# Optimization experiments

Hardware: AMD Instinct MI355X
Metric: run time of the kernel (lower is better)

Reference implementation:

```python
import jax, jax.numpy as jnp
import numpy as np
from jax import lax

KERNEL = 3
SAMPLING_RATE = 100.0
N_GRID = 201  # np.linspace(-1, 1, 201) sub-sample grid


def setup_inputs() -> dict:
    key = jax.random.key(0)
    nb, nc, nx, nt = 32, 3, 64, 4096
    xcorr = jax.random.normal(key, (nb, nc, nx, nt), dtype=jnp.float32)
    return {"xcorr": xcorr, "nlag": nt // 2}


def reference(xcorr, nlag):
    nt = xcorr.shape[-1]
    x = jnp.abs(xcorr)  # vabs=True

    # max_pool2d with (1, kernel=3), stride 1, padding (0, 1) -> SAME max over lag axis
    smax = lax.reduce_window(
        x, -jnp.inf, lax.max,
        window_dimensions=(1, 1, 1, KERNEL),
        window_strides=(1, 1, 1, 1),
        padding=[(0, 0), (0, 0), (0, 0), (KERNEL // 2, KERNEL // 2)],
    )
    keep = (smax == x).astype(x.dtype)

    # top-2 local maxima along lag axis (sorted descending, like torch.topk)
    topk_score, topk_idx = lax.top_k(x * keep, 2)
    s0 = topk_score[..., 0]
    s1 = topk_score[..., 1]
    weight = (0.1 + 3.0 * (s0 - s1)) * s0 ** 2
    i0 = topk_idx[..., 0]  # [nb, nc, nx]

    # --- sub-sample interpolation: 3-point spline == parabola through neighbors ---
    offsets = jnp.array([-1, 0, 1], dtype=i0.dtype)
    nbr_idx = jnp.clip(i0[..., None] + offsets, 0, nt - 1)      # [nb,nc,nx,3]
    y = jnp.take_along_axis(x, nbr_idx, axis=-1)                 # [nb,nc,nx,3]
    ym1, y0, yp1 = y[..., 0], y[..., 1], y[..., 2]
    a = 0.5 * (ym1 + yp1) - y0   # quadratic coeff
    b = 0.5 * (yp1 - ym1)        # linear coeff
    c = y0                       # constant

    xg = jnp.linspace(-1.0, 1.0, N_GRID, dtype=x.dtype)          # [201]
    yg = (a[..., None] * xg + b[..., None]) * xg + c[..., None]  # [nb,nc,nx,201]
    ii = jnp.argmax(yg, axis=-1)                                  # [nb,nc,nx]
    sub_shift = xg[ii]
    topk_idx_f = i0.astype(x.dtype) + sub_shift
    topk_score0 = jnp.take_along_axis(yg, ii[..., None], axis=-1)[..., 0]

    # pick the channel with the largest weight
    idx = jnp.argmax(weight, axis=1, keepdims=True)               # [nb,1,nx]
    max_cc = jnp.take_along_axis(topk_score0, idx, axis=1)
    w = jnp.take_along_axis(weight, idx, axis=1)
    shift_idx = jnp.take_along_axis(topk_idx_f, idx, axis=1) - jnp.asarray(nlag, x.dtype)
    shift_t = shift_idx / SAMPLING_RATE

    # stacked: [cc_max, cc_weight, cc_dt, cc_shift], each [nb,1,nx]
    return jnp.stack([max_cc, w, shift_t, shift_idx], axis=0)
```

## Files before the change

### kernel.cpp

```cpp
#include <hip/hip_runtime.h>
#include <math.h>

#define NB 32
#define NC 3
#define NX 64
#define NT 4096
#define NROWS (NB * NC * NX)
#define NGRID 201

__device__ __forceinline__ bool better(float va, int ia, float vb, int ib) {
    return (va > vb) || (va == vb && ia < ib);
}

__global__ __launch_bounds__(256) void row_peaks_kernel(
    const float* __restrict__ xcorr,
    float* __restrict__ w_out,
    float* __restrict__ s_out,
    float* __restrict__ f_out)
{
    __shared__ float xs[NT];
    __shared__ float rv0[4], rv1[4];
    __shared__ int   ri0[4], ri1[4];

    const int row = blockIdx.x;
    const int tid = threadIdx.x;
    const float* __restrict__ xr = xcorr + (size_t)row * NT;

    #pragma unroll
    for (int it = 0; it < NT / 1024; ++it) {
        const int e = it * 1024 + tid * 4;
        float4 v = *reinterpret_cast<const float4*>(xr + e);
        xs[e + 0] = fabsf(v.x);
        xs[e + 1] = fabsf(v.y);
        xs[e + 2] = fabsf(v.z);
        xs[e + 3] = fabsf(v.w);
    }
    __syncthreads();

    float v0 = -1.0f, v1 = -1.0f;
    int   i0 = 0x7fffffff, i1 = 0x7fffffff;
    #pragma unroll
    for (int it = 0; it < NT / 256; ++it) {
        const int t = it * 256 + tid;
        const float c = xs[t];
        const float l = (t > 0)      ? xs[t - 1] : -INFINITY;
        const float r = (t < NT - 1) ? xs[t + 1] : -INFINITY;
        const float v = (c >= l && c >= r) ? c : 0.0f;
        if (v > v0)      { v1 = v0; i1 = i0; v0 = v; i0 = t; }
        else if (v > v1) { v1 = v;  i1 = t; }
    }

    #pragma unroll
    for (int off = 1; off < 64; off <<= 1) {
        const float ov0 = __shfl_xor(v0, off);
        const int   oi0 = __shfl_xor(i0, off);
        const float ov1 = __shfl_xor(v1, off);
        const int   oi1 = __shfl_xor(i1, off);
        if (better(ov0, oi0, v0, i0)) {
            float nv1; int ni1;
            if (better(v0, i0, ov1, oi1)) { nv1 = v0;  ni1 = i0;  }
            else                          { nv1 = ov1; ni1 = oi1; }
            v0 = ov0; i0 = oi0; v1 = nv1; i1 = ni1;
        } else {
            if (better(ov0, oi0, v1, i1)) { v1 = ov0; i1 = oi0; }
        }
    }

    const int wid = tid >> 6;
    if ((tid & 63) == 0) { rv0[wid] = v0; ri0[wid] = i0; rv1[wid] = v1; ri1[wid] = i1; }
    __syncthreads();

    if (tid < 64) {
        float a0 = rv0[0], a1 = rv1[0];
        int   ai0 = ri0[0], ai1 = ri1[0];
        #pragma unroll
        for (int w = 1; w < 4; ++w) {
            const float b0 = rv0[w], b1 = rv1[w];
            const int   bi0 = ri0[w], bi1 = ri1[w];
            if (better(b0, bi0, a0, ai0)) {
                float nv1; int ni1;
                if (better(a0, ai0, b1, bi1)) { nv1 = a0; ni1 = ai0; }
                else                          { nv1 = b1; ni1 = bi1; }
                a0 = b0; ai0 = bi0; a1 = nv1; ai1 = ni1;
            } else {
                if (better(b0, bi0, a1, ai1)) { a1 = b0; ai1 = bi0; }
            }
        }

        const float s0 = a0, s1 = a1;
        const int   p0 = ai0;
        const float s0sq   = s0 * s0;
        const float weight = (0.1f + 3.0f * (s0 - s1)) * s0sq;

        const int im1 = (p0 - 1 < 0) ? 0 : p0 - 1;
        const int ip1 = (p0 + 1 > NT - 1) ? NT - 1 : p0 + 1;
        const float ym1 = xs[im1], yc = xs[p0], yp1 = xs[ip1];
        const float A = 0.5f * (ym1 + yp1) - yc;
        const float B = 0.5f * (yp1 - ym1);
        const float C = yc;

        float bv = -INFINITY; int bi = 0x7fffffff;
        #pragma unroll
        for (int k = 0; k < 4; ++k) {
            const int gi = tid + k * 64;
            if (gi < NGRID) {
                const float xg = 0.01f * (float)(gi - 100);
                const float yg = (A * xg + B) * xg + C;
                if (yg > bv) { bv = yg; bi = gi; }
            }
        }
        #pragma unroll
        for (int off = 1; off < 64; off <<= 1) {
            const float ov = __shfl_xor(bv, off);
            const int   oi = __shfl_xor(bi, off);
            if (ov > bv || (ov == bv && oi < bi)) { bv = ov; bi = oi; }
        }

        if (tid == 0) {
            const float sub = 0.01f * (float)(bi - 100);
            w_out[row] = weight;
            s_out[row] = bv;
            f_out[row] = (float)p0 + sub;
        }
    }
}

__global__ __launch_bounds__(256) void select_channel_kernel(
    const float* __restrict__ w_in,
    const float* __restrict__ s_in,
    const float* __restrict__ f_in,
    const int*   __restrict__ nlag_p,
    float* __restrict__ out)
{
    const int idx = blockIdx.x * blockDim.x + threadIdx.x;
    const int n = NB * NX;
    if (idx >= n) return;
    const int b = idx / NX;
    const int x = idx % NX;

    const float nlagf = (float)(*nlag_p);

    float bw = -INFINITY; int bc = 0;
    #pragma unroll
    for (int c = 0; c < NC; ++c) {
        const float wc = w_in[(b * NC + c) * NX + x];
        if (wc > bw) { bw = wc; bc = c; }
    }
    const int rsel = (b * NC + bc) * NX + x;
    const float mc = s_in[rsel];
    const float shift_idx = f_in[rsel] - nlagf;

    const int o = b * NX + x;
    out[0 * n + o] = mc;
    out[1 * n + o] = bw;
    out[2 * n + o] = shift_idx / 100.0f;
    out[3 * n + o] = shift_idx;
}

extern "C" void kernel_launch(void* const* d_in, const int* in_sizes, int n_in,
                              void* d_out, int out_size, void* d_ws, size_t ws_size,
                              hipStream_t stream) {
    const float* xcorr  = (const float*)d_in[0];
    const int*   nlag_p = (const int*)d_in[1];
    float* out = (float*)d_out;

    float* ws = (float*)d_ws;
    float* w_buf = ws;
    float* s_buf = ws + NROWS;
    float* f_buf = ws + 2 * NROWS;

    row_peaks_kernel<<<NROWS, 256, 0, stream>>>(xcorr, w_buf, s_buf, f_buf);

    const int n2 = NB * NX;
    select_channel_kernel<<<(n2 + 255) / 256, 256, 0, stream>>>(
        w_buf, s_buf, f_buf, nlag_p, out);
}
```

Baseline: 27.69 us.

## Fuse channel selection into peak kernel and replace LDS staging with shuffles

Merges the per-row peak kernel and the channel-selection kernel into one kernel where each block handles all three channels of a (batch, x) position and writes the final outputs directly. The row is no longer staged in shared memory; neighbours for the local-max test come from wave shuffles plus boundary loads, and interpolation neighbours are reread from global memory. This removes a kernel launch and the workspace round trip, but cuts the grid to a third and serialises the three channels within each block with extra barriers.

```diff
diff --git a/kernel.cpp b/kernel.cpp
--- a/kernel.cpp
+++ b/kernel.cpp
@@ -5,156 +5,148 @@
 #define NC 3
 #define NX 64
 #define NT 4096
-#define NROWS (NB * NC * NX)
 #define NGRID 201
 
 __device__ __forceinline__ bool better(float va, int ia, float vb, int ib) {
     return (va > vb) || (va == vb && ia < ib);
 }
 
-__global__ __launch_bounds__(256) void row_peaks_kernel(
+__global__ __launch_bounds__(256) void detect_peaks_kernel(
     const float* __restrict__ xcorr,
-    float* __restrict__ w_out,
-    float* __restrict__ s_out,
-    float* __restrict__ f_out)
+    const int*   __restrict__ nlag_p,
+    float* __restrict__ out)
 {
-    __shared__ float xs[NT];
     __shared__ float rv0[4], rv1[4];
     __shared__ int   ri0[4], ri1[4];
 
-    const int row = blockIdx.x;
-    const int tid = threadIdx.x;
-    const float* __restrict__ xr = xcorr + (size_t)row * NT;
+    const int bid  = blockIdx.x;
+    const int b    = bid / NX;
+    const int x    = bid % NX;
+    const int tid  = threadIdx.x;
+    const int lane = tid & 63;
+    const int wid  = tid >> 6;
 
-    #pragma unroll
-    for (int it = 0; it < NT / 1024; ++it) {
-        const int e = it * 1024 + tid * 4;
-        float4 v = *reinterpret_cast<const float4*>(xr + e);
-        xs[e + 0] = fabsf(v.x);
-        xs[e + 1] = fabsf(v.y);
-        xs[e + 2] = fabsf(v.z);
-        xs[e + 3] = fabsf(v.w);
-    }
-    __syncthreads();
+    float best_w = -INFINITY, best_s = 0.0f, best_f = 0.0f;
 
-    float v0 = -1.0f, v1 = -1.0f;
-    int   i0 = 0x7fffffff, i1 = 0x7fffffff;
-    #pragma unroll
-    for (int it = 0; it < NT / 256; ++it) {
-        const int t = it * 256 + tid;
-        const float c = xs[t];
-        const float l = (t > 0)      ? xs[t - 1] : -INFINITY;
-        const float r = (t < NT - 1) ? xs[t + 1] : -INFINITY;
-        const float v = (c >= l && c >= r) ? c : 0.0f;
-        if (v > v0)      { v1 = v0; i1 = i0; v0 = v; i0 = t; }
-        else if (v > v1) { v1 = v;  i1 = t; }
-    }
+    for (int c = 0; c < NC; ++c) {
+        const float* __restrict__ xr =
+            xcorr + ((size_t)((b * NC + c) * NX) + x) * NT;
 
-    #pragma unroll
-    for (int off = 1; off < 64; off <<= 1) {
-        const float ov0 = __shfl_xor(v0, off);
-        const int   oi0 = __shfl_xor(i0, off);
-        const float ov1 = __shfl_xor(v1, off);
-        const int   oi1 = __shfl_xor(i1, off);
-        if (better(ov0, oi0, v0, i0)) {
-            float nv1; int ni1;
-            if (better(v0, i0, ov1, oi1)) { nv1 = v0;  ni1 = i0;  }
-            else                          { nv1 = ov1; ni1 = oi1; }
-            v0 = ov0; i0 = oi0; v1 = nv1; i1 = ni1;
-        } else {
-            if (better(ov0, oi0, v1, i1)) { v1 = ov0; i1 = oi0; }
+        float v0 = -1.0f, v1 = -1.0f;
+        int   i0 = 0x7fffffff, i1 = 0x7fffffff;
+
+        #pragma unroll
+        for (int k = 0; k < 4; ++k) {
+            const int t4 = (k * 256 + tid) * 4;
+            const float4 v = *reinterpret_cast<const float4*>(xr + t4);
+            const float a0 = fabsf(v.x), a1 = fabsf(v.y);
+            const float a2 = fabsf(v.z), a3 = fabsf(v.w);
+
+            float lm = __shfl_up(a3, 1);
+            float rm = __shfl_down(a0, 1);
+            if (lane == 0)  lm = (t4 > 0)      ? fabsf(xr[t4 - 1]) : -INFINITY;
+            if (lane == 63) rm = (t4 + 4 < NT) ? fabsf(xr[t4 + 4]) : -INFINITY;
+
+            const float c0 = (a0 >= lm && a0 >= a1) ? a0 : 0.0f;
+            const float c1 = (a1 >= a0 && a1 >= a2) ? a1 : 0.0f;
+            const float c2 = (a2 >= a1 && a2 >= a3) ? a2 : 0.0f;
+            const float c3 = (a3 >= a2 && a3 >= rm) ? a3 : 0.0f;
+
+            if (c0 > v0)      { v1 = v0; i1 = i0; v0 = c0; i0 = t4;     }
+            else if (c0 > v1) { v1 = c0; i1 = t4;                       }
+            if (c1 > v0)      { v1 = v0; i1 = i0; v0 = c1; i0 = t4 + 1; }
+            else if (c1 > v1) { v1 = c1; i1 = t4 + 1;                   }
+            if (c2 > v0)      { v1 = v0; i1 = i0; v0 = c2; i0 = t4 + 2; }
+            else if (c2 > v1) { v1 = c2; i1 = t4 + 2;                   }
+            if (c3 > v0)      { v1 = v0; i1 = i0; v0 = c3; i0 = t4 + 3; }
+            else if (c3 > v1) { v1 = c3; i1 = t4 + 3;                   }
         }
-    }
 
-    const int wid = tid >> 6;
-    if ((tid & 63) == 0) { rv0[wid] = v0; ri0[wid] = i0; rv1[wid] = v1; ri1[wid] = i1; }
-    __syncthreads();
-
-    if (tid < 64) {
-        float a0 = rv0[0], a1 = rv1[0];
-        int   ai0 = ri0[0], ai1 = ri1[0];
         #pragma unroll
-        for (int w = 1; w < 4; ++w) {
-            const float b0 = rv0[w], b1 = rv1[w];
-            const int   bi0 = ri0[w], bi1 = ri1[w];
-            if (better(b0, bi0, a0, ai0)) {
+        for (int off = 1; off < 64; off <<= 1) {
+            const float ov0 = __shfl_xor(v0, off);
+            const int   oi0 = __shfl_xor(i0, off);
+            const float ov1 = __shfl_xor(v1, off);
+            const int   oi1 = __shfl_xor(i1, off);
+            if (better(ov0, oi0, v0, i0)) {
                 float nv1; int ni1;
-                if (better(a0, ai0, b1, bi1)) { nv1 = a0; ni1 = ai0; }
-                else                          { nv1 = b1; ni1 = bi1; }
-                a0 = b0; ai0 = bi0; a1 = nv1; ai1 = ni1;
+                if (better(v0, i0, ov1, oi1)) { nv1 = v0;  ni1 = i0;  }
+                else                          { nv1 = ov1; ni1 = oi1; }
+                v0 = ov0; i0 = oi0; v1 = nv1; i1 = ni1;
             } else {
-                if (better(b0, bi0, a1, ai1)) { a1 = b0; ai1 = bi0; }
+                if (better(ov0, oi0, v1, i1)) { v1 = ov0; i1 = oi0; }
             }
         }
 
-        const float s0 = a0, s1 = a1;
-        const int   p0 = ai0;
-        const float s0sq   = s0 * s0;
-        const float weight = (0.1f + 3.0f * (s0 - s1)) * s0sq;
+        if (lane == 0) { rv0[wid] = v0; ri0[wid] = i0; rv1[wid] = v1; ri1[wid] = i1; }
+        __syncthreads();
 
-        const int im1 = (p0 - 1 < 0) ? 0 : p0 - 1;
-        const int ip1 = (p0 + 1 > NT - 1) ? NT - 1 : p0 + 1;
-        const float ym1 = xs[im1], yc = xs[p0], yp1 = xs[ip1];
-        const float A = 0.5f * (ym1 + yp1) - yc;
-        const float B = 0.5f * (yp1 - ym1);
-        const float C = yc;
+        if (tid < 64) {
+            float a0 = rv0[0], a1 = rv1[0];
+            int   ai0 = ri0[0], ai1 = ri1[0];
+            #pragma unroll
+            for (int w = 1; w < 4; ++w) {
+                const float b0 = rv0[w], b1 = rv1[w];
+                const int   bi0 = ri0[w], bi1 = ri1[w];
+                if (better(b0, bi0, a0, ai0)) {
+                    float nv1; int ni1;
+                    if (better(a0, ai0, b1, bi1)) { nv1 = a0; ni1 = ai0; }
+                    else                          { nv1 = b1; ni1 = bi1; }
+                    a0 = b0; ai0 = bi0; a1 = nv1; ai1 = ni1;
+                } else {
+                    if (better(b0, bi0, a1, ai1)) { a1 = b0; ai1 = bi0; }
+                }
+            }
 
-        float bv = -INFINITY; int bi = 0x7fffffff;
-        #pragma unroll
-        for (int k = 0; k < 4; ++k) {
-            const int gi = tid + k * 64;
-            if (gi < NGRID) {
-                const float xg = 0.01f * (float)(gi - 100);
-                const float yg = (A * xg + B) * xg + C;
-                if (yg > bv) { bv = yg; bi = gi; }
+            const float s0 = a0, s1 = a1;
+            const int   p0 = ai0;
+            const float weight = (0.1f + 3.0f * (s0 - s1)) * (s0 * s0);
+
+            const int im1 = (p0 - 1 < 0) ? 0 : p0 - 1;
+            const int ip1 = (p0 + 1 > NT - 1) ? NT - 1 : p0 + 1;
+            const float ym1 = fabsf(xr[im1]);
+            const float yc  = fabsf(xr[p0]);
+            const float yp1 = fabsf(xr[ip1]);
+            const float A = 0.5f * (ym1 + yp1) - yc;
+            const float B = 0.5f * (yp1 - ym1);
+            const float C = yc;
+
+            float bv = -INFINITY; int bi = 0x7fffffff;
+            #pragma unroll
+            for (int k = 0; k < 4; ++k) {
+                const int gi = lane + k * 64;
+                if (gi < NGRID) {
+                    const float xg = 0.01f * (float)(gi - 100);
+                    const float yg = (A * xg + B) * xg + C;
+                    if (yg > bv) { bv = yg; bi = gi; }
+                }
+            }
+            #pragma unroll
+            for (int off = 1; off < 64; off <<= 1) {
+                const float ov = __shfl_xor(bv, off);
+                const int   oi = __shfl_xor(bi, off);
+                if (ov > bv || (ov == bv && oi < bi)) { bv = ov; bi = oi; }
+            }
+
+            if (weight > best_w) {
+                best_w = weight;
+                best_s = bv;
+                best_f = (float)p0 + 0.01f * (float)(bi - 100);
             }
         }
-        #pragma unroll
-        for (int off = 1; off < 64; off <<= 1) {
-            const float ov = __shfl_xor(bv, off);
-            const int   oi = __shfl_xor(bi, off);
-            if (ov > bv || (ov == bv && oi < bi)) { bv = ov; bi = oi; }
-        }
+        __syncthreads();
+    }
 
-        if (tid == 0) {
-            const float sub = 0.01f * (float)(bi - 100);
-            w_out[row] = weight;
-            s_out[row] = bv;
-            f_out[row] = (float)p0 + sub;
-        }
+    if (tid == 0) {
+        const float nlagf = (float)(*nlag_p);
+        const int n = NB * NX;
+        const int o = b * NX + x;
+        const float shift_idx = best_f - nlagf;
+        out[0 * n + o] = best_s;
+        out[1 * n + o] = best_w;
+        out[2 * n + o] = shift_idx / 100.0f;
+        out[3 * n + o] = shift_idx;
     }
-}
-
-__global__ __launch_bounds__(256) void select_channel_kernel(
-    const float* __restrict__ w_in,
-    const float* __restrict__ s_in,
-    const float* __restrict__ f_in,
-    const int*   __restrict__ nlag_p,
-    float* __restrict__ out)
-{
-    const int idx = blockIdx.x * blockDim.x + threadIdx.x;
-    const int n = NB * NX;
-    if (idx >= n) return;
-    const int b = idx / NX;
-    const int x = idx % NX;
-
-    const float nlagf = (float)(*nlag_p);
-
-    float bw = -INFINITY; int bc = 0;
-    #pragma unroll
-    for (int c = 0; c < NC; ++c) {
-        const float wc = w_in[(b * NC + c) * NX + x];
-        if (wc > bw) { bw = wc; bc = c; }
-    }
-    const int rsel = (b * NC + bc) * NX + x;
-    const float mc = s_in[rsel];
-    const float shift_idx = f_in[rsel] - nlagf;
-
-    const int o = b * NX + x;
-    out[0 * n + o] = mc;
-    out[1 * n + o] = bw;
-    out[2 * n + o] = shift_idx / 100.0f;
-    out[3 * n + o] = shift_idx;
 }
 
 extern "C" void kernel_launch(void* const* d_in, const int* in_sizes, int n_in,
@@ -164,14 +156,5 @@
     const int*   nlag_p = (const int*)d_in[1];
     float* out = (float*)d_out;
 
-    float* ws = (float*)d_ws;
-    float* w_buf = ws;
-    float* s_buf = ws + NROWS;
-    float* f_buf = ws + 2 * NROWS;
-
-    row_peaks_kernel<<<NROWS, 256, 0, stream>>>(xcorr, w_buf, s_buf, f_buf);
-
-    const int n2 = NB * NX;
-    select_channel_kernel<<<(n2 + 255) / 256, 256, 0, stream>>>(
-        w_buf, s_buf, f_buf, nlag_p, out);
+    detect_peaks_kernel<<<NB * NX, 256, 0, stream>>>(xcorr, nlag_p, out);
 }
```

After: 29.26 us. +5.7%, slower.
